# Optimization experiments

Measured on AMD Instinct MI355X. Metric: run time of the kernel, lower is better.

The kernel has to match this reference:

```python
import jax, jax.numpy as jnp
import numpy as np

EMB = 1024
NH = 16
DH = EMB // NH
SCALE = np.sqrt(EMB).astype(np.float32)  # module scales by sqrt(emb_dim), not sqrt(d_head)


def setup_inputs() -> dict:
    key = jax.random.key(0)
    ks = jax.random.split(key, 9)
    s = 1.0 / np.sqrt(EMB)
    return {
        "a": jax.random.normal(ks[0], (4, 2048, EMB), jnp.float32),
        "Wq": jax.random.normal(ks[1], (EMB, EMB), jnp.float32) * s,
        "bq": jnp.zeros((EMB,), jnp.float32),
        "Wk": jax.random.normal(ks[2], (EMB, EMB), jnp.float32) * s,
        "bk": jnp.zeros((EMB,), jnp.float32),
        "Wv": jax.random.normal(ks[3], (EMB, EMB), jnp.float32) * s,
        "bv": jnp.zeros((EMB,), jnp.float32),
        "Wo": jax.random.normal(ks[4], (EMB, EMB), jnp.float32) * s,
        "bo": jnp.zeros((EMB,), jnp.float32),
    }


def reference(a, Wq, bq, Wk, bk, Wv, bv, Wo, bo):
    N, S, _ = a.shape
    # Q/K/V projections (self-attention: b is None -> b = a)
    Q = (a @ Wq + bq).reshape(N, S, NH, DH).transpose(0, 2, 1, 3)  # [N,H,A,D]
    K = (a @ Wk + bk).reshape(N, S, NH, DH).transpose(0, 2, 1, 3)  # [N,H,B,D]
    V = (a @ Wv + bv).reshape(N, S, NH, DH).transpose(0, 2, 1, 3)  # [N,H,B,D]
    score = jnp.einsum('nhad,nhbd->nhab', Q, K) / SCALE
    score = jax.nn.softmax(score, axis=-1)
    out = jnp.einsum('nhab,nhbd->nhad', score, V)                  # [N,H,A,D]
    out = out.transpose(0, 2, 1, 3).reshape(N, S, EMB)
    return out @ Wo + bo
```

## Files before the change

### kernel.cpp

```cpp
#include <hip/hip_runtime.h>
#include <hip/hip_bf16.h>
#include <stdint.h>

typedef __attribute__((ext_vector_type(8))) short short8v;
typedef __attribute__((ext_vector_type(4))) float float4v;

#define GLDS16(gp, lp) __builtin_amdgcn_global_load_lds( \
    (const __attribute__((address_space(1))) void*)(gp),  \
    (__attribute__((address_space(3))) void*)(lp), 16, 0, 0)

#if __has_builtin(__builtin_amdgcn_exp2f)
#define EXP2(x) __builtin_amdgcn_exp2f(x)
#else
#define EXP2(x) exp2f(x)
#endif

#define LOG2E 1.4426950408889634f

__global__ __launch_bounds__(256) void cast_a_kernel(
    const float* __restrict__ src, __hip_bfloat16* __restrict__ dst, int n4) {
  int i = blockIdx.x * blockDim.x + threadIdx.x;
  if (i < n4) {
    float4 v = ((const float4*)src)[i];
    union { __hip_bfloat16 h[4]; ushort4 u; } p;
    p.h[0] = __float2bfloat16(v.x);
    p.h[1] = __float2bfloat16(v.y);
    p.h[2] = __float2bfloat16(v.z);
    p.h[3] = __float2bfloat16(v.w);
    ((ushort4*)dst)[i] = p.u;
  }
}

__global__ __launch_bounds__(256) void transpose4_kernel(
    const float* __restrict__ Wq, const float* __restrict__ Wk,
    const float* __restrict__ Wv, const float* __restrict__ Wo,
    __hip_bfloat16* __restrict__ Wcat, __hip_bfloat16* __restrict__ WoT) {
  __shared__ float t[32][33];
  const int z = blockIdx.z;
  const float* W = (z == 0) ? Wq : (z == 1) ? Wk : (z == 2) ? Wv : Wo;
  __hip_bfloat16* dst = (z < 3) ? (Wcat + (size_t)z * 1048576) : WoT;
  int tx = threadIdx.x & 31, ty = threadIdx.x >> 5;
  int r0 = blockIdx.y * 32, c0 = blockIdx.x * 32;
#pragma unroll
  for (int i = 0; i < 4; ++i) {
    int r = ty + i * 8;
    t[r][tx] = W[(size_t)(r0 + r) * 1024 + c0 + tx];
  }
  __syncthreads();
#pragma unroll
  for (int i = 0; i < 4; ++i) {
    int r = ty + i * 8;
    dst[(size_t)(c0 + r) * 1024 + r0 + tx] = __float2bfloat16(t[tx][r]);
  }
}

__global__ __launch_bounds__(256, 2) void gemm_qkv_kernel(
    const __hip_bfloat16* __restrict__ A, const __hip_bfloat16* __restrict__ BT,
    const float* __restrict__ bq, const float* __restrict__ bk,
    const float* __restrict__ bv, __hip_bfloat16* __restrict__ Qh,
    __hip_bfloat16* __restrict__ Kh, __hip_bfloat16* __restrict__ Vt) {
  __shared__ char lds[32768];
  const int tid = threadIdx.x;
  const int l = tid & 63, w = tid >> 6;
  const int g = l >> 4, cc = l & 15;
  const int bid = blockIdx.x;
  const int nbid = (bid & 7) * 192 + (bid >> 3);
  const int m0 = (nbid & 63) * 128, n0 = (nbid >> 6) * 128;
  const int wm = w >> 1, wn = w & 1;

  float4v acc[4][4];
#pragma unroll
  for (int m = 0; m < 4; ++m)
#pragma unroll
    for (int n = 0; n < 4; ++n) acc[m][n] = (float4v){0.f, 0.f, 0.f, 0.f};

  for (int kt = 0; kt < 16; ++kt) {
#pragma unroll
    for (int j = 0; j < 4; ++j) {
      int ci = (w * 4 + j) * 64 + l;
      int row = ci >> 3, ko = (ci & 7) * 16;
      GLDS16((const char*)A + (size_t)(m0 + row) * 2048 + kt * 128 + ko,
             lds + ci * 16);
      GLDS16((const char*)BT + (size_t)(n0 + row) * 2048 + kt * 128 + ko,
             lds + 16384 + ci * 16);
    }
    __syncthreads();
#pragma unroll
    for (int h = 0; h < 2; ++h) {
      short8v af[4], bf[4];
#pragma unroll
      for (int m = 0; m < 4; ++m)
        af[m] = *(const short8v*)(lds + (wm * 64 + m * 16 + cc) * 128 + h * 64 + g * 16);
#pragma unroll
      for (int n = 0; n < 4; ++n)
        bf[n] = *(const short8v*)(lds + 16384 + (wn * 64 + n * 16 + cc) * 128 + h * 64 + g * 16);
#pragma unroll
      for (int m = 0; m < 4; ++m)
#pragma unroll
        for (int n = 0; n < 4; ++n)
          acc[m][n] = __builtin_amdgcn_mfma_f32_16x16x32_bf16(af[m], bf[n], acc[m][n], 0, 0, 0);
    }
    __syncthreads();
  }

  const int sec = n0 >> 10;
  if (sec < 2) {
    __hip_bfloat16* out = sec == 0 ? Qh : Kh;
    const float* bias = sec == 0 ? bq : bk;
    const float scale = sec == 0 ? (LOG2E / 32.f) : 1.f;
#pragma unroll
    for (int m = 0; m < 4; ++m) {
#pragma unroll
      for (int n = 0; n < 4; ++n) {
        int colc = (n0 + wn * 64 + n * 16 + cc) & 1023;
        float b = bias[colc];
        int h = colc >> 6, d = colc & 63;
#pragma unroll
        for (int r = 0; r < 4; ++r) {
          int grow = m0 + wm * 64 + m * 16 + g * 4 + r;
          int nb = grow >> 11, s = grow & 2047;
          out[((size_t)(nb * 16 + h) * 2048 + s) * 64 + d] =
              __float2bfloat16((acc[m][n][r] + b) * scale);
        }
      }
    }
  } else {
#pragma unroll
    for (int m = 0; m < 4; ++m) {
      int grow0 = m0 + wm * 64 + m * 16 + g * 4;
      int nb = grow0 >> 11, key0 = grow0 & 2047;
      int kp0 = (key0 & ~31) | ((key0 & 12) << 1) | (((key0 >> 4) & 1) << 2);
#pragma unroll
      for (int n = 0; n < 4; ++n) {
        int colc = (n0 + wn * 64 + n * 16 + cc) & 1023;
        float b = bv[colc];
        int h = colc >> 6, d = colc & 63;
        union { __hip_bfloat16 h4[4]; uint2 u; } pk;
#pragma unroll
        for (int r = 0; r < 4; ++r) pk.h4[r] = __float2bfloat16(acc[m][n][r] + b);
        *(uint2*)&Vt[((size_t)((nb * 16 + h) * 64 + d)) * 2048 + kp0] = pk.u;
      }
    }
  }
}

__global__ __launch_bounds__(256, 2) void gemm_o_kernel(
    const __hip_bfloat16* __restrict__ A, const __hip_bfloat16* __restrict__ BT,
    const float* __restrict__ bias, float* __restrict__ C) {
  __shared__ char lds[32768];
  const int tid = threadIdx.x;
  const int l = tid & 63, w = tid >> 6;
  const int g = l >> 4, cc = l & 15;
  const int bid = blockIdx.x;
  const int nbid = (bid & 7) * 64 + (bid >> 3);
  const int m0 = (nbid & 63) * 128, n0 = (nbid >> 6) * 128;
  const int wm = w >> 1, wn = w & 1;

  float4v acc[4][4];
#pragma unroll
  for (int m = 0; m < 4; ++m)
#pragma unroll
    for (int n = 0; n < 4; ++n) acc[m][n] = (float4v){0.f, 0.f, 0.f, 0.f};

  for (int kt = 0; kt < 16; ++kt) {
#pragma unroll
    for (int j = 0; j < 4; ++j) {
      int ci = (w * 4 + j) * 64 + l;
      int row = ci >> 3, ko = (ci & 7) * 16;
      GLDS16((const char*)A + (size_t)(m0 + row) * 2048 + kt * 128 + ko,
             lds + ci * 16);
      GLDS16((const char*)BT + (size_t)(n0 + row) * 2048 + kt * 128 + ko,
             lds + 16384 + ci * 16);
    }
    __syncthreads();
#pragma unroll
    for (int h = 0; h < 2; ++h) {
      short8v af[4], bf[4];
#pragma unroll
      for (int m = 0; m < 4; ++m)
        af[m] = *(const short8v*)(lds + (wm * 64 + m * 16 + cc) * 128 + h * 64 + g * 16);
#pragma unroll
      for (int n = 0; n < 4; ++n)
        bf[n] = *(const short8v*)(lds + 16384 + (wn * 64 + n * 16 + cc) * 128 + h * 64 + g * 16);
#pragma unroll
      for (int m = 0; m < 4; ++m)
#pragma unroll
        for (int n = 0; n < 4; ++n)
          acc[m][n] = __builtin_amdgcn_mfma_f32_16x16x32_bf16(af[m], bf[n], acc[m][n], 0, 0, 0);
    }
    __syncthreads();
  }

#pragma unroll
  for (int m = 0; m < 4; ++m) {
    int row = m0 + wm * 64 + m * 16 + g * 4;
#pragma unroll
    for (int n = 0; n < 4; ++n) {
      int col = n0 + wn * 64 + n * 16 + cc;
      float b = bias[col];
#pragma unroll
      for (int r = 0; r < 4; ++r)
        C[(size_t)(row + r) * 1024 + col] = acc[m][n][r] + b;
    }
  }
}

__global__ __launch_bounds__(512, 4) void attn_kernel(
    const __hip_bfloat16* __restrict__ Q,
    const __hip_bfloat16* __restrict__ K,
    const __hip_bfloat16* __restrict__ VT,
    __hip_bfloat16* __restrict__ AO) {
  __shared__ char sK[3][8192];
  __shared__ char sV[3][8192];
  const int tid = threadIdx.x;
  const int l = tid & 63, w = tid >> 6;
  const int g = l >> 4, cc = l & 15;
  const int bid = blockIdx.x;
  const int nbid = (bid & 7) * 64 + (bid >> 3);
  const int bx = nbid & 7, nh = nbid >> 3;
  const int q0 = bx * 256 + w * 32;
  const char* Kb = (const char*)(K + (size_t)nh * 131072);
  const char* Vb = (const char*)(VT + (size_t)nh * 131072);
  const __hip_bfloat16* Qb = Q + (size_t)nh * 131072;

  short8v qf[2][2];
#pragma unroll
  for (int qg = 0; qg < 2; ++qg)
#pragma unroll
    for (int dh = 0; dh < 2; ++dh)
      qf[qg][dh] = *(const short8v*)(Qb + (size_t)(q0 + qg * 16 + cc) * 64 + dh * 32 + g * 8);

  int koff[4][2], voff[4][2];
#pragma unroll
  for (int kg = 0; kg < 4; ++kg)
#pragma unroll
    for (int dh = 0; dh < 2; ++dh) {
      int row = kg * 16 + cc;
      koff[kg][dh] = (row * 128 + dh * 64 + g * 16) ^ ((row & 7) << 4);
    }
#pragma unroll
  for (int f = 0; f < 4; ++f)
#pragma unroll
    for (int hh = 0; hh < 2; ++hh) {
      int d = f * 16 + cc;
      voff[f][hh] = (d * 128 + hh * 64 + g * 16) ^ ((d & 7) << 4);
    }
  const int ss = tid * 16;
  const int sr = ss >> 7;
  const int soff = (ss & 127) ^ ((sr & 7) << 4);
  const int stKo = sr * 128 + soff;
  const int stVo = sr * 4096 + soff;

  const short8v fone = {16256, 16256, 16256, 16256, 16256, 16256, 16256, 16256};

  float lr[2] = {0.f, 0.f};
  float4v oacc[2][4];
#pragma unroll
  for (int qg = 0; qg < 2; ++qg)
#pragma unroll
    for (int f = 0; f < 4; ++f) oacc[qg][f] = (float4v){0.f, 0.f, 0.f, 0.f};

#define STAGE(kb, vb, ktv)                                                    \
  {                                                                           \
    GLDS16(Kb + (size_t)(ktv) * 8192 + stKo, (kb) + ss);                      \
    GLDS16(Vb + (size_t)(ktv) * 128 + stVo, (vb) + ss);                       \
  }

  char *k0 = sK[0], *k1 = sK[1], *k2 = sK[2];
  char *v0 = sV[0], *v1 = sV[1], *v2 = sV[2];
  STAGE(k0, v0, 0);
  STAGE(k1, v1, 1);

  for (int kt = 0; kt < 32; ++kt) {
    if (kt < 31) {
      asm volatile("s_waitcnt vmcnt(2)" ::: "memory");
    } else {
      asm volatile("s_waitcnt vmcnt(0)" ::: "memory");
    }
    __builtin_amdgcn_s_barrier();
    if (kt < 30) STAGE(k2, v2, kt + 2);
    const char* sKc = k0;
    const char* sVc = v0;

    short8v kf[4][2];
#pragma unroll
    for (int kg = 0; kg < 4; ++kg)
#pragma unroll
      for (int dh = 0; dh < 2; ++dh)
        kf[kg][dh] = *(const short8v*)(sKc + koff[kg][dh]);

    float4v sv[2][4];
    __builtin_amdgcn_s_setprio(1);
#pragma unroll
    for (int qg = 0; qg < 2; ++qg)
#pragma unroll
      for (int kg = 0; kg < 4; ++kg) {
        float4v z = (float4v){0.f, 0.f, 0.f, 0.f};
        z = __builtin_amdgcn_mfma_f32_16x16x32_bf16(kf[kg][0], qf[qg][0], z, 0, 0, 0);
        sv[qg][kg] = __builtin_amdgcn_mfma_f32_16x16x32_bf16(kf[kg][1], qf[qg][1], z, 0, 0, 0);
      }
    __builtin_amdgcn_s_setprio(0);

    short8v pf[2][2];
#pragma unroll
    for (int qg = 0; qg < 2; ++qg) {
#pragma unroll
      for (int kg = 0; kg < 4; ++kg)
#pragma unroll
        for (int r = 0; r < 4; ++r) sv[qg][kg][r] = EXP2(sv[qg][kg][r]);
#pragma unroll
      for (int hh = 0; hh < 2; ++hh) {
        union { __hip_bfloat16 h[8]; short8v v8; } pk;
#pragma unroll
        for (int j = 0; j < 4; ++j) {
          pk.h[j]     = __float2bfloat16(sv[qg][2 * hh][j]);
          pk.h[4 + j] = __float2bfloat16(sv[qg][2 * hh + 1][j]);
        }
        pf[qg][hh] = pk.v8;
      }
      float4v t = (float4v){0.f, 0.f, 0.f, 0.f};
      t = __builtin_amdgcn_mfma_f32_16x16x32_bf16(fone, pf[qg][0], t, 0, 0, 0);
      t = __builtin_amdgcn_mfma_f32_16x16x32_bf16(fone, pf[qg][1], t, 0, 0, 0);
      lr[qg] += t[0];
    }

    __builtin_amdgcn_s_setprio(1);
#pragma unroll
    for (int f = 0; f < 4; ++f)
#pragma unroll
      for (int hh = 0; hh < 2; ++hh) {
        short8v vk = *(const short8v*)(sVc + voff[f][hh]);
#pragma unroll
        for (int qg = 0; qg < 2; ++qg)
          oacc[qg][f] = __builtin_amdgcn_mfma_f32_16x16x32_bf16(vk, pf[qg][hh], oacc[qg][f], 0, 0, 0);
      }
    __builtin_amdgcn_s_setprio(0);

    char* tt;
    tt = k0; k0 = k1; k1 = k2; k2 = tt;
    tt = v0; v0 = v1; v1 = v2; v2 = tt;
  }
#undef STAGE

  int nb = nh >> 4, h = nh & 15;
#pragma unroll
  for (int qg = 0; qg < 2; ++qg) {
    float inv = 1.f / lr[qg];
    int qrow = q0 + qg * 16 + cc;
#pragma unroll
    for (int f = 0; f < 4; ++f)
#pragma unroll
      for (int r = 0; r < 4; ++r) {
        int d = f * 16 + g * 4 + r;
        AO[(size_t)(nb * 2048 + qrow) * 1024 + h * 64 + d] =
            __float2bfloat16(oacc[qg][f][r] * inv);
      }
  }
}

extern "C" void kernel_launch(void* const* d_in, const int* in_sizes, int n_in,
                              void* d_out, int out_size, void* d_ws, size_t ws_size,
                              hipStream_t stream) {
  const float* a  = (const float*)d_in[0];
  const float* Wq = (const float*)d_in[1];
  const float* bq = (const float*)d_in[2];
  const float* Wk = (const float*)d_in[3];
  const float* bk = (const float*)d_in[4];
  const float* Wv = (const float*)d_in[5];
  const float* bv = (const float*)d_in[6];
  const float* Wo = (const float*)d_in[7];
  const float* bo = (const float*)d_in[8];

  char* ws = (char*)d_ws;
  __hip_bfloat16* aB   = (__hip_bfloat16*)(ws);
  __hip_bfloat16* Wcat = (__hip_bfloat16*)(ws + (16ull << 20));
  __hip_bfloat16* WoT  = (__hip_bfloat16*)(ws + (22ull << 20));
  __hip_bfloat16* Qh   = (__hip_bfloat16*)(ws + (24ull << 20));
  __hip_bfloat16* Kh   = (__hip_bfloat16*)(ws + (40ull << 20));
  __hip_bfloat16* Vt   = (__hip_bfloat16*)(ws + (56ull << 20));
  __hip_bfloat16* AOb  = (__hip_bfloat16*)(ws + (72ull << 20));

  cast_a_kernel<<<8192, 256, 0, stream>>>(a, aB, 8192 * 1024 / 4);
  dim3 tg(32, 32, 4);
  transpose4_kernel<<<tg, 256, 0, stream>>>(Wq, Wk, Wv, Wo, Wcat, WoT);

  gemm_qkv_kernel<<<1536, 256, 0, stream>>>(aB, Wcat, bq, bk, bv, Qh, Kh, Vt);

  attn_kernel<<<512, 512, 0, stream>>>(Qh, Kh, Vt, AOb);

  gemm_o_kernel<<<512, 256, 0, stream>>>(AOb, WoT, bo, (float*)d_out);
}
```

Baseline: 187.6 us.

## Rewrite QKV GEMM as 256x256-tile 8-wave kernel with double-buffered swizzled LDS

Replaces the 128x128 single-buffered QKV projection GEMM with a 256x256 tile kernel using 8 waves, 128KB of double-buffered LDS, XOR-swizzled LDS addressing and interleaved global-to-LDS loads with MFMA phases. The aim is to hide global load latency behind compute, avoid LDS bank conflicts and raise data reuse per tile. In exchange, each workgroup needs far more LDS and registers, and only 384 workgroups are launched, which may hurt occupancy and wave balance across CUs.

```diff
diff --git a/kernel.cpp b/kernel.cpp
--- a/kernel.cpp
+++ b/kernel.cpp
@@ -54,54 +54,105 @@
   }
 }
 
-__global__ __launch_bounds__(256, 2) void gemm_qkv_kernel(
+__global__ __launch_bounds__(512, 2) void gemm_qkv8_kernel(
     const __hip_bfloat16* __restrict__ A, const __hip_bfloat16* __restrict__ BT,
     const float* __restrict__ bq, const float* __restrict__ bk,
     const float* __restrict__ bv, __hip_bfloat16* __restrict__ Qh,
     __hip_bfloat16* __restrict__ Kh, __hip_bfloat16* __restrict__ Vt) {
-  __shared__ char lds[32768];
+  __shared__ char lds[131072];
   const int tid = threadIdx.x;
   const int l = tid & 63, w = tid >> 6;
   const int g = l >> 4, cc = l & 15;
+  const int wm = w >> 2, wn = w & 3;
+  const int sw = (cc & 7) << 4;
   const int bid = blockIdx.x;
-  const int nbid = (bid & 7) * 192 + (bid >> 3);
-  const int m0 = (nbid & 63) * 128, n0 = (nbid >> 6) * 128;
-  const int wm = w >> 1, wn = w & 1;
-
-  float4v acc[4][4];
-#pragma unroll
-  for (int m = 0; m < 4; ++m)
+  const int nbid = (bid & 7) * 48 + (bid >> 3);
+  const int tm = nbid / 12, tn = nbid % 12;
+  const int m0 = tm * 256, n0 = tn * 256;
+
+  const int scol = ((tid & 7) * 16) ^ (((tid >> 3) & 7) << 4);
+  const char* pA = (const char*)A + (size_t)(m0 + (tid >> 3)) * 2048 + scol;
+  const char* pB = (const char*)BT + (size_t)(n0 + (tid >> 3)) * 2048 + scol;
+  char* ldsT = lds + tid * 16;
+
+#define STGH(pG, base, half, kt) {                                            \
+    GLDS16((pG) + ((half) * 128) * 2048 + (kt) * 128,                         \
+           ldsT + (base) + (half) * 16384);                                   \
+    GLDS16((pG) + ((half) * 128 + 64) * 2048 + (kt) * 128,                    \
+           ldsT + (base) + (half) * 16384 + 8192);                            \
+  }
+
+  short8v af[4][2], bf[4][2];
+#define DSA(base, fmb)                                                        \
+  _Pragma("unroll") for (int i = 0; i < 4; ++i)                               \
+  _Pragma("unroll") for (int kk = 0; kk < 2; ++kk)                            \
+    af[i][kk] = *(const short8v*)(lds + (base) +                              \
+        (((wm * 128 + ((fmb) + i) * 16 + cc) * 128 + kk * 64 + g * 16) ^ sw));
+#define DSB(base, np)                                                         \
+  _Pragma("unroll") for (int ii = 0; ii < 2; ++ii)                            \
+  _Pragma("unroll") for (int kk = 0; kk < 2; ++kk)                            \
+    bf[(np) * 2 + ii][kk] = *(const short8v*)(lds + (base) +                  \
+        (((wn * 64 + ((np) * 2 + ii) * 16 + cc) * 128 + kk * 64 + g * 16) ^ sw));
+
+  float4v acc[8][4];
+#pragma unroll
+  for (int m = 0; m < 8; ++m)
 #pragma unroll
     for (int n = 0; n < 4; ++n) acc[m][n] = (float4v){0.f, 0.f, 0.f, 0.f};
 
-  for (int kt = 0; kt < 16; ++kt) {
-#pragma unroll
-    for (int j = 0; j < 4; ++j) {
-      int ci = (w * 4 + j) * 64 + l;
-      int row = ci >> 3, ko = (ci & 7) * 16;
-      GLDS16((const char*)A + (size_t)(m0 + row) * 2048 + kt * 128 + ko,
-             lds + ci * 16);
-      GLDS16((const char*)BT + (size_t)(n0 + row) * 2048 + kt * 128 + ko,
-             lds + 16384 + ci * 16);
-    }
-    __syncthreads();
-#pragma unroll
-    for (int h = 0; h < 2; ++h) {
-      short8v af[4], bf[4];
-#pragma unroll
-      for (int m = 0; m < 4; ++m)
-        af[m] = *(const short8v*)(lds + (wm * 64 + m * 16 + cc) * 128 + h * 64 + g * 16);
-#pragma unroll
-      for (int n = 0; n < 4; ++n)
-        bf[n] = *(const short8v*)(lds + 16384 + (wn * 64 + n * 16 + cc) * 128 + h * 64 + g * 16);
-#pragma unroll
-      for (int m = 0; m < 4; ++m)
-#pragma unroll
-        for (int n = 0; n < 4; ++n)
-          acc[m][n] = __builtin_amdgcn_mfma_f32_16x16x32_bf16(af[m], bf[n], acc[m][n], 0, 0, 0);
-    }
-    __syncthreads();
-  }
+#define MM(fmb, np)                                                           \
+  __builtin_amdgcn_s_setprio(1);                                              \
+  _Pragma("unroll") for (int i = 0; i < 4; ++i)                               \
+  _Pragma("unroll") for (int ii = 0; ii < 2; ++ii)                            \
+  _Pragma("unroll") for (int kk = 0; kk < 2; ++kk)                            \
+    acc[(fmb) + i][(np) * 2 + ii] = __builtin_amdgcn_mfma_f32_16x16x32_bf16(  \
+        af[i][kk], bf[(np) * 2 + ii][kk], acc[(fmb) + i][(np) * 2 + ii], 0, 0, 0); \
+  __builtin_amdgcn_s_setprio(0);
+
+#define BAR() __builtin_amdgcn_s_barrier()
+#define WAIT4() asm volatile("s_waitcnt vmcnt(4)" ::: "memory")
+
+  STGH(pB, 65536, 0, 0); STGH(pB, 65536, 1, 0);
+  STGH(pA, 0, 0, 0);     STGH(pA, 0, 1, 0);
+  STGH(pB, 98304, 0, 1); STGH(pB, 98304, 1, 1);
+  WAIT4();
+  BAR();
+
+  for (int j = 0; j < 8; ++j) {
+    const int vv = 2 * j + 1;
+    const int u2 = (j < 7) ? 2 * j + 2 : 15;
+    const int v2 = (j < 7) ? 2 * j + 3 : 15;
+    DSA(0, 0); DSB(65536, 0);
+    STGH(pA, 32768, 0, vv);
+    BAR(); MM(0, 0); BAR();
+    DSB(65536, 1);
+    STGH(pA, 32768, 1, vv);
+    BAR(); MM(0, 1); BAR();
+    DSA(0, 4);
+    STGH(pB, 65536, 0, u2);
+    BAR(); MM(4, 0); BAR();
+    STGH(pB, 65536, 1, u2);
+    WAIT4();
+    BAR(); MM(4, 1); BAR();
+    DSA(32768, 0); DSB(98304, 0);
+    STGH(pA, 0, 0, u2);
+    BAR(); MM(0, 0); BAR();
+    DSB(98304, 1);
+    STGH(pA, 0, 1, u2);
+    BAR(); MM(0, 1); BAR();
+    DSA(32768, 4);
+    STGH(pB, 98304, 0, v2);
+    BAR(); MM(4, 0); BAR();
+    STGH(pB, 98304, 1, v2);
+    WAIT4();
+    BAR(); MM(4, 1); BAR();
+  }
+#undef STGH
+#undef DSA
+#undef DSB
+#undef MM
+#undef BAR
+#undef WAIT4
 
   const int sec = n0 >> 10;
   if (sec < 2) {
@@ -109,7 +160,7 @@
     const float* bias = sec == 0 ? bq : bk;
     const float scale = sec == 0 ? (LOG2E / 32.f) : 1.f;
 #pragma unroll
-    for (int m = 0; m < 4; ++m) {
+    for (int m = 0; m < 8; ++m) {
 #pragma unroll
       for (int n = 0; n < 4; ++n) {
         int colc = (n0 + wn * 64 + n * 16 + cc) & 1023;
@@ -117,7 +168,7 @@
         int h = colc >> 6, d = colc & 63;
 #pragma unroll
         for (int r = 0; r < 4; ++r) {
-          int grow = m0 + wm * 64 + m * 16 + g * 4 + r;
+          int grow = m0 + wm * 128 + m * 16 + g * 4 + r;
           int nb = grow >> 11, s = grow & 2047;
           out[((size_t)(nb * 16 + h) * 2048 + s) * 64 + d] =
               __float2bfloat16((acc[m][n][r] + b) * scale);
@@ -126,8 +177,8 @@
     }
   } else {
 #pragma unroll
-    for (int m = 0; m < 4; ++m) {
-      int grow0 = m0 + wm * 64 + m * 16 + g * 4;
+    for (int m = 0; m < 8; ++m) {
+      int grow0 = m0 + wm * 128 + m * 16 + g * 4;
       int nb = grow0 >> 11, key0 = grow0 & 2047;
       int kp0 = (key0 & ~31) | ((key0 & 12) << 1) | (((key0 >> 4) & 1) << 2);
 #pragma unroll
@@ -384,7 +435,7 @@
   dim3 tg(32, 32, 4);
   transpose4_kernel<<<tg, 256, 0, stream>>>(Wq, Wk, Wv, Wo, Wcat, WoT);
 
-  gemm_qkv_kernel<<<1536, 256, 0, stream>>>(aB, Wcat, bq, bk, bv, Qh, Kh, Vt);
+  gemm_qkv8_kernel<<<384, 512, 0, stream>>>(aB, Wcat, bq, bk, bv, Qh, Kh, Vt);
 
   attn_kernel<<<512, 512, 0, stream>>>(Qh, Kh, Vt, AOb);
 
```

Measured after the change: 177.8 us. -5.2%, faster.
